# Kernel tuning notes

Hardware: AMD Instinct MI355X
Metric: run time of the kernel (lower is better)

## Reference

```python
import jax, jax.numpy as jnp
import numpy as np

UP = jnp.array([0.0, 1.0, 0.0], dtype=jnp.float32)
LEASH = 15.0


def q_inv(q):
    return jnp.concatenate([-q[..., :3], q[..., 3:]], axis=-1)


def q_mul(q1, q2):
    x1, y1, z1, w1 = q1[..., 0], q1[..., 1], q1[..., 2], q1[..., 3]
    x2, y2, z2, w2 = q2[..., 0], q2[..., 1], q2[..., 2], q2[..., 3]
    return jnp.stack([
        w1 * x2 + x1 * w2 + y1 * z2 - z1 * y2,
        w1 * y2 - x1 * z2 + y1 * w2 + z1 * x2,
        w1 * z2 + x1 * y2 - y1 * x2 + z1 * w2,
        w1 * w2 - x1 * x2 - y1 * y2 - z1 * z2], axis=-1)


def q_rot(q, v):
    qv, qw = q[..., :3], q[..., 3:]
    t = 2.0 * jnp.cross(qv, v)
    return v + qw * t + jnp.cross(qv, t)


def mat_to_quat(R):
    # Batched [E,3,3] -> [E,4] (x,y,z,w), matching the torch branch structure.
    r = lambda i, j: R[:, i, j]
    eps = 1e-12
    tr = r(0, 0) + r(1, 1) + r(2, 2)
    Sa = jnp.sqrt(jnp.maximum(tr + 1.0, eps)) * 2.0
    qa = jnp.stack([(r(2, 1) - r(1, 2)) / Sa, (r(0, 2) - r(2, 0)) / Sa,
                    (r(1, 0) - r(0, 1)) / Sa, 0.25 * Sa], -1)
    Sb = jnp.sqrt(jnp.maximum(1.0 + r(0, 0) - r(1, 1) - r(2, 2), eps)) * 2.0
    qb = jnp.stack([0.25 * Sb, (r(0, 1) + r(1, 0)) / Sb,
                    (r(0, 2) + r(2, 0)) / Sb, (r(2, 1) - r(1, 2)) / Sb], -1)
    Sc = jnp.sqrt(jnp.maximum(1.0 + r(1, 1) - r(0, 0) - r(2, 2), eps)) * 2.0
    qc = jnp.stack([(r(0, 1) + r(1, 0)) / Sc, 0.25 * Sc,
                    (r(1, 2) + r(2, 1)) / Sc, (r(0, 2) - r(2, 0)) / Sc], -1)
    Sd = jnp.sqrt(jnp.maximum(1.0 + r(2, 2) - r(0, 0) - r(1, 1), eps)) * 2.0
    qd = jnp.stack([(r(0, 2) + r(2, 0)) / Sd, (r(1, 2) + r(2, 1)) / Sd,
                    0.25 * Sd, (r(1, 0) - r(0, 1)) / Sd], -1)
    cond_b = ((r(0, 0) > r(1, 1)) & (r(0, 0) > r(2, 2)))[:, None]
    cond_c = (r(1, 1) > r(2, 2))[:, None]
    return jnp.where((tr > 0)[:, None], qa,
                     jnp.where(cond_b, qb, jnp.where(cond_c, qc, qd)))


def sfm_pose_loss(pred_t, pred_q, gt_t, gt_q, batch_counts):
    E = batch_counts.shape[0]
    N = pred_t.shape[0]
    counts = batch_counts.astype(jnp.float32)  # [E]
    seg = jnp.repeat(jnp.arange(E), batch_counts, total_repeat_length=N)  # [N]
    starts = jnp.cumsum(batch_counts) - batch_counts  # first index of each episode
    sseg = lambda x: jax.ops.segment_sum(x, seg, num_segments=E)

    # --- per-episode centering ---
    mu_p = sseg(pred_t) / counts[:, None]
    mu_g = sseg(gt_t) / counts[:, None]
    p_c = pred_t - mu_p[seg]
    g_c = gt_t - mu_g[seg]

    # degenerate episodes: too short or near-zero gt variance (unbiased var)
    g_var = sseg(jnp.sum(g_c ** 2, -1)) / (counts - 1.0)
    deg = (batch_counts < 4) | (g_var < 1e-4)  # [E]

    # --- Umeyama: batched 3x3 SVD of H = p_c^T @ g_c per episode ---
    H = sseg(p_c[:, :, None] * g_c[:, None, :])  # [E,3,3]
    H_safe = jnp.where(deg[:, None, None], jnp.diag(jnp.array([3.0, 2.0, 1.0])), H)
    U, S, Vh = jnp.linalg.svd(H_safe, full_matrices=False)
    V = jnp.swapaxes(Vh, -1, -2)
    R0 = jnp.einsum('eij,ekj->eik', V, U)  # V @ U^T
    sgn = jnp.where(jnp.linalg.det(R0) < 0, -1.0, 1.0)
    V_adj = V * jnp.stack([jnp.ones_like(sgn), jnp.ones_like(sgn), sgn], -1)[:, None, :]
    R = jnp.einsum('eij,ekj->eik', V_adj, U)  # [E,3,3]

    p_rot = jnp.einsum('nij,nj->ni', R[seg], p_c)
    denom = sseg(jnp.sum(p_c ** 2, -1))
    nom = sseg(jnp.sum(p_rot * g_c, -1))
    s = jnp.where(denom > 1e-6,
                  jnp.clip(nom / jnp.maximum(denom, 1e-6), 1e-3, 1e3), 1.0)

    # --- translation loss (per-episode mse, then mean over episodes) ---
    p_al = jnp.where(deg[seg][:, None], p_c, p_rot * s[seg][:, None])
    diff = p_al - g_c
    loss_trans = jnp.mean(sseg(jnp.sum(diff ** 2, -1)) / (counts * 3.0))

    # --- scale loss (only non-degenerate episodes) ---
    loss_scale = jnp.sum(jnp.where(deg, 0.0, jnp.log(jnp.abs(s) + 1e-6) ** 2)) / E

    # --- rotation loss ---
    q_align = mat_to_quat(R)  # [E,4]
    q0_p = pred_q[starts]
    q0_g = gt_q[starts]
    pq_deg = q_mul(q_inv(q0_p)[seg], pred_q)
    gq_deg = q_mul(q_inv(q0_g)[seg], gt_q)
    pq_ume = q_mul(q_align[seg], pred_q)
    dm = deg[seg][:, None]
    pq_al = jnp.where(dm, pq_deg, pq_ume)
    gq_al = jnp.where(dm, gq_deg, gt_q)
    dot = jnp.sum(pq_al * gq_al, -1)
    loss_rot = jnp.mean(sseg(1.0 - dot ** 2) / counts)

    # --- gravity loss ---
    up = jnp.broadcast_to(UP, pred_q.shape[:-1] + (3,))
    pu = q_rot(q_inv(pred_q), up)
    gu = q_rot(q_inv(gt_q), up)
    cos = jnp.sum(pu * gu, -1) / jnp.maximum(
        jnp.linalg.norm(pu, axis=-1) * jnp.linalg.norm(gu, axis=-1), 1e-8)
    loss_grav = jnp.mean(sseg(1.0 - cos) / counts)

    # --- frame0 leash (deadzone on first translation of each episode) ---
    mag = jnp.linalg.norm(pred_t[starts], axis=-1)
    loss_leash = jnp.mean(jnp.maximum(mag - LEASH, 0.0) ** 2)

    return jnp.stack([loss_trans, loss_rot, loss_grav, loss_leash, loss_scale])


def setup_inputs() -> dict:
    rng = np.random.default_rng(0)
    E = 4096
    counts = rng.integers(64, 449, size=E)
    counts[:8] = np.array([2, 3, 3, 2, 3, 2, 3, 3])  # exercise degenerate branch
    N = int(counts.sum())
    key = jax.random.key(0)
    k1, k2, k3, k4 = jax.random.split(key, 4)
    pred_t = jax.random.normal(k1, (N, 3), dtype=jnp.float32) * 5.0
    gt_t = jax.random.normal(k2, (N, 3), dtype=jnp.float32) * 5.0

    def rand_unit_quat(k):
        q = jax.random.normal(k, (N, 4), dtype=jnp.float32)
        return q / jnp.linalg.norm(q, axis=-1, keepdims=True)

    return {
        'pred_t': pred_t,
        'pred_q': rand_unit_quat(k3),
        'gt_t': gt_t,
        'gt_q': rand_unit_quat(k4),
        'batch_counts': jnp.asarray(counts, dtype=jnp.int32),
    }


def reference(pred_t, pred_q, gt_t, gt_q, batch_counts):
    # Returns [loss_trans, loss_rot, loss_grav, loss_leash, loss_scale]
    return sfm_pose_loss(pred_t, pred_q, gt_t, gt_q, batch_counts)
```

## Files before the change

### kernel.cpp

```cpp
#include <hip/hip_runtime.h>
#include <math.h>

__global__ void scan_kernel(const int* __restrict__ counts,
                            int* __restrict__ starts, int E) {
    __shared__ int lds[1024];
    int tid = threadIdx.x;
    int base = tid * 4;
    int c0 = (base + 0 < E) ? counts[base + 0] : 0;
    int c1 = (base + 1 < E) ? counts[base + 1] : 0;
    int c2 = (base + 2 < E) ? counts[base + 2] : 0;
    int c3 = (base + 3 < E) ? counts[base + 3] : 0;
    lds[tid] = c0 + c1 + c2 + c3;
    __syncthreads();
    for (int off = 1; off < 1024; off <<= 1) {
        int v = lds[tid];
        int a = (tid >= off) ? lds[tid - off] : 0;
        __syncthreads();
        lds[tid] = v + a;
        __syncthreads();
    }
    int excl = (tid > 0) ? lds[tid - 1] : 0;
    if (base + 0 < E) starts[base + 0] = excl; excl += c0;
    if (base + 1 < E) starts[base + 1] = excl; excl += c1;
    if (base + 2 < E) starts[base + 2] = excl; excl += c2;
    if (base + 3 < E) starts[base + 3] = excl;
}

__device__ __forceinline__ float4 qmul4(float4 a, float4 b) {
    return make_float4(
        a.w*b.x + a.x*b.w + a.y*b.z - a.z*b.y,
        a.w*b.y - a.x*b.z + a.y*b.w + a.z*b.x,
        a.w*b.z + a.x*b.y - a.y*b.x + a.z*b.w,
        a.w*b.w - a.x*b.x - a.y*b.y - a.z*b.z);
}

__device__ __forceinline__ void qinv_rot_up(float4 q, float out[3]) {
    float qx = -q.x, qy = -q.y, qz = -q.z, qw = q.w;
    float tx = -2.f*qz;
    float ty = 0.f;
    float tz = 2.f*qx;
    out[0] = 0.f + qw*tx + (qy*tz - qz*ty);
    out[1] = 1.f + qw*ty + (qz*tx - qx*tz);
    out[2] = 0.f + qw*tz + (qx*ty - qy*tx);
}

__device__ __forceinline__ float wave_sum(float v) {
    v += __shfl_xor(v, 32);
    v += __shfl_xor(v, 16);
    v += __shfl_xor(v, 8);
    v += __shfl_xor(v, 4);
    v += __shfl_xor(v, 2);
    v += __shfl_xor(v, 1);
    return v;
}

__device__ void jacobi3f(float A[3][3], float V[3][3]) {
    V[0][0]=1.f; V[0][1]=0.f; V[0][2]=0.f;
    V[1][0]=0.f; V[1][1]=1.f; V[1][2]=0.f;
    V[2][0]=0.f; V[2][1]=0.f; V[2][2]=1.f;
    for (int sweep = 0; sweep < 6; ++sweep) {
        float off = A[0][1]*A[0][1] + A[0][2]*A[0][2] + A[1][2]*A[1][2];
        float dia = A[0][0]*A[0][0] + A[1][1]*A[1][1] + A[2][2]*A[2][2];
        if (off <= 1e-12f * (dia + 1e-30f)) break;
        for (int p = 0; p < 2; ++p) for (int q = p + 1; q < 3; ++q) {
            float apq = A[p][q];
            if (fabsf(apq) < 1e-30f) continue;
            float theta = (A[q][q] - A[p][p]) / (2.0f * apq);
            float t = ((theta >= 0.f) ? 1.f : -1.f) / (fabsf(theta) + sqrtf(theta*theta + 1.f));
            float cc = 1.f / sqrtf(t*t + 1.f);
            float ss = t * cc;
            float app = A[p][p], aqq = A[q][q];
            A[p][p] = app - t * apq;
            A[q][q] = aqq + t * apq;
            A[p][q] = 0.f; A[q][p] = 0.f;
            int r = 3 - p - q;
            float arp = A[r][p], arq = A[r][q];
            A[r][p] = cc*arp - ss*arq; A[p][r] = A[r][p];
            A[r][q] = ss*arp + cc*arq; A[q][r] = A[r][q];
            for (int i = 0; i < 3; ++i) {
                float vip = V[i][p], viq = V[i][q];
                V[i][p] = cc*vip - ss*viq;
                V[i][q] = ss*vip + cc*viq;
            }
        }
    }
}

__device__ void mat2quatf(const float R[3][3], float q[4]) {
    const float eps = 1e-12f;
    float tr = R[0][0] + R[1][1] + R[2][2];
    if (tr > 0.f) {
        float S = sqrtf(fmaxf(tr + 1.f, eps)) * 2.f;
        q[0] = (R[2][1]-R[1][2])/S; q[1] = (R[0][2]-R[2][0])/S;
        q[2] = (R[1][0]-R[0][1])/S; q[3] = 0.25f*S;
    } else if ((R[0][0] > R[1][1]) && (R[0][0] > R[2][2])) {
        float S = sqrtf(fmaxf(1.f + R[0][0] - R[1][1] - R[2][2], eps)) * 2.f;
        q[0] = 0.25f*S; q[1] = (R[0][1]+R[1][0])/S;
        q[2] = (R[0][2]+R[2][0])/S; q[3] = (R[2][1]-R[1][2])/S;
    } else if (R[1][1] > R[2][2]) {
        float S = sqrtf(fmaxf(1.f + R[1][1] - R[0][0] - R[2][2], eps)) * 2.f;
        q[0] = (R[0][1]+R[1][0])/S; q[1] = 0.25f*S;
        q[2] = (R[1][2]+R[2][1])/S; q[3] = (R[0][2]-R[2][0])/S;
    } else {
        float S = sqrtf(fmaxf(1.f + R[2][2] - R[0][0] - R[1][1], eps)) * 2.f;
        q[0] = (R[0][2]+R[2][0])/S; q[1] = (R[1][2]+R[2][1])/S;
        q[2] = 0.25f*S; q[3] = (R[1][0]-R[0][1])/S;
    }
}

#define NS 29
__global__ __launch_bounds__(256) void fused_kernel(
    const float* __restrict__ pred_t, const float4* __restrict__ pred_q,
    const float* __restrict__ gt_t,   const float4* __restrict__ gt_q,
    const int* __restrict__ counts, const int* __restrict__ starts,
    float* __restrict__ segloss, int E)
{
    int e = blockIdx.x;
    int tid = threadIdx.x;
    int lane = tid & 63;
    int wv = tid >> 6;
    int start = starts[e];
    int ci = counts[e];
    float4 q0p = pred_q[start];
    float4 q0g = gt_q[start];
    float4 q0pi = make_float4(-q0p.x, -q0p.y, -q0p.z, q0p.w);
    float4 q0gi = make_float4(-q0g.x, -q0g.y, -q0g.z, q0g.w);
    float t0x = pred_t[3*start+0], t0y = pred_t[3*start+1], t0z = pred_t[3*start+2];
    bool small_c = (ci < 4);

    float acc[NS];
    #pragma unroll
    for (int k = 0; k < NS; ++k) acc[k] = 0.f;

    for (int i = tid; i < ci; i += 256) {
        int n = start + i;
        float px = pred_t[3*n+0], py = pred_t[3*n+1], pz = pred_t[3*n+2];
        float gx = gt_t[3*n+0],  gy = gt_t[3*n+1],  gz = gt_t[3*n+2];
        float4 pq = pred_q[n];
        float4 gq = gt_q[n];

        acc[0] += px; acc[1] += py; acc[2] += pz;
        acc[3] += gx; acc[4] += gy; acc[5] += gz;
        acc[6] += px*px + py*py + pz*pz;
        acc[7] += gx*gx + gy*gy + gz*gz;
        acc[8]  += px*gx; acc[9]  += px*gy; acc[10] += px*gz;
        acc[11] += py*gx; acc[12] += py*gy; acc[13] += py*gz;
        acc[14] += pz*gx; acc[15] += pz*gy; acc[16] += pz*gz;

        float mx =  pq.w*gq.x - pq.z*gq.y + pq.y*gq.z - pq.x*gq.w;
        float my =  pq.z*gq.x + pq.w*gq.y - pq.x*gq.z - pq.y*gq.w;
        float mz = -pq.y*gq.x + pq.x*gq.y + pq.w*gq.z - pq.z*gq.w;
        float mw =  pq.x*gq.x + pq.y*gq.y + pq.z*gq.z + pq.w*gq.w;
        acc[17] += mx*mx; acc[18] += mx*my; acc[19] += mx*mz; acc[20] += mx*mw;
        acc[21] += my*my; acc[22] += my*mz; acc[23] += my*mw;
        acc[24] += mz*mz; acc[25] += mz*mw; acc[26] += mw*mw;

        float pu[3], gu[3];
        qinv_rot_up(pq, pu);
        qinv_rot_up(gq, gu);
        float cosv = pu[0]*gu[0] + pu[1]*gu[1] + pu[2]*gu[2];
        acc[27] += 1.f - cosv;

        if (small_c) {
            float4 aa = qmul4(q0pi, pq);
            float4 bb = qmul4(q0gi, gq);
            float dd = aa.x*bb.x + aa.y*bb.y + aa.z*bb.z + aa.w*bb.w;
            acc[28] += 1.f - dd*dd;
        }
    }

    #pragma unroll
    for (int k = 0; k < NS; ++k) acc[k] = wave_sum(acc[k]);

    __shared__ float red[4][NS];
    if (lane == 0) {
        #pragma unroll
        for (int k = 0; k < NS; ++k) red[wv][k] = acc[k];
    }
    __syncthreads();
    if (wv != 0) return;

    float A[NS];
    #pragma unroll
    for (int k = 0; k < NS; ++k)
        A[k] = red[0][k] + red[1][k] + red[2][k] + red[3][k];

    float c = (float)ci;
    float mu_p[3] = { A[0]/c, A[1]/c, A[2]/c };
    float mu_g[3] = { A[3]/c, A[4]/c, A[5]/c };
    float pp_c = A[6] - c*(mu_p[0]*mu_p[0]+mu_p[1]*mu_p[1]+mu_p[2]*mu_p[2]);
    float gg_c = A[7] - c*(mu_g[0]*mu_g[0]+mu_g[1]*mu_g[1]+mu_g[2]*mu_g[2]);
    float H[3][3];
    H[0][0]=A[8] -c*mu_p[0]*mu_g[0]; H[0][1]=A[9] -c*mu_p[0]*mu_g[1]; H[0][2]=A[10]-c*mu_p[0]*mu_g[2];
    H[1][0]=A[11]-c*mu_p[1]*mu_g[0]; H[1][1]=A[12]-c*mu_p[1]*mu_g[1]; H[1][2]=A[13]-c*mu_p[1]*mu_g[2];
    H[2][0]=A[14]-c*mu_p[2]*mu_g[0]; H[2][1]=A[15]-c*mu_p[2]*mu_g[1]; H[2][2]=A[16]-c*mu_p[2]*mu_g[2];
    float g_var = gg_c / (c - 1.0f);
    bool deg = small_c || (g_var < 1e-4f);
    float trans, rot, scale = 0.f;
    if (deg) {
        float s28;
        if (small_c) {
            s28 = A[28];
        } else {
            float local = 0.f;
            for (int i = lane; i < ci; i += 64) {
                int n = start + i;
                float4 aa = qmul4(q0pi, pred_q[n]);
                float4 bb = qmul4(q0gi, gt_q[n]);
                float dd = aa.x*bb.x + aa.y*bb.y + aa.z*bb.z + aa.w*bb.w;
                local += 1.f - dd*dd;
            }
            s28 = wave_sum(local);
        }
        float trH = H[0][0] + H[1][1] + H[2][2];
        trans = (pp_c - 2.f*trH + gg_c) / (c * 3.f);
        rot = s28 / c;
    } else {
        float B[3][3], V[3][3];
        for (int i = 0; i < 3; ++i)
            for (int j = 0; j < 3; ++j)
                B[i][j] = H[0][i]*H[0][j] + H[1][i]*H[1][j] + H[2][i]*H[2][j];
        jacobi3f(B, V);
        float lam[3] = { B[0][0], B[1][1], B[2][2] };
        int idx[3] = {0, 1, 2};
        if (lam[idx[0]] < lam[idx[1]]) { int t = idx[0]; idx[0] = idx[1]; idx[1] = t; }
        if (lam[idx[0]] < lam[idx[2]]) { int t = idx[0]; idx[0] = idx[2]; idx[2] = t; }
        if (lam[idx[1]] < lam[idx[2]]) { int t = idx[1]; idx[1] = idx[2]; idx[2] = t; }
        float v1[3], v2[3], v3[3];
        for (int i = 0; i < 3; ++i) { v1[i] = V[i][idx[0]]; v2[i] = V[i][idx[1]]; v3[i] = V[i][idx[2]]; }
        float detV = v1[0]*(v2[1]*v3[2]-v2[2]*v3[1])
                   - v1[1]*(v2[0]*v3[2]-v2[2]*v3[0])
                   + v1[2]*(v2[0]*v3[1]-v2[1]*v3[0]);
        float sgnV = (detV < 0.f) ? -1.f : 1.f;
        float u1[3], u2[3], u3[3];
        for (int i = 0; i < 3; ++i) u1[i] = H[i][0]*v1[0] + H[i][1]*v1[1] + H[i][2]*v1[2];
        float n1 = fmaxf(sqrtf(u1[0]*u1[0]+u1[1]*u1[1]+u1[2]*u1[2]), 1e-30f);
        for (int i = 0; i < 3; ++i) u1[i] /= n1;
        for (int i = 0; i < 3; ++i) u2[i] = H[i][0]*v2[0] + H[i][1]*v2[1] + H[i][2]*v2[2];
        float d12 = u1[0]*u2[0]+u1[1]*u2[1]+u1[2]*u2[2];
        for (int i = 0; i < 3; ++i) u2[i] -= d12*u1[i];
        float n2 = fmaxf(sqrtf(u2[0]*u2[0]+u2[1]*u2[1]+u2[2]*u2[2]), 1e-30f);
        for (int i = 0; i < 3; ++i) u2[i] /= n2;
        u3[0] = u1[1]*u2[2] - u1[2]*u2[1];
        u3[1] = u1[2]*u2[0] - u1[0]*u2[2];
        u3[2] = u1[0]*u2[1] - u1[1]*u2[0];
        float R[3][3];
        for (int i = 0; i < 3; ++i)
            for (int k = 0; k < 3; ++k)
                R[i][k] = v1[i]*u1[k] + v2[i]*u2[k] + sgnV*v3[i]*u3[k];
        float nom = 0.f;
        for (int k = 0; k < 3; ++k)
            for (int j = 0; j < 3; ++j)
                nom += R[k][j] * H[j][k];
        float denom = pp_c;
        float s = 1.f;
        if (denom > 1e-6f) {
            s = nom / fmaxf(denom, 1e-6f);
            s = fminf(fmaxf(s, 1e-3f), 1e3f);
        }
        trans = (s*s*denom - 2.f*s*nom + gg_c) / (c * 3.f);
        float ls = logf(fabsf(s) + 1e-6f);
        scale = ls * ls;
        float q[4];
        mat2quatf(R, q);
        float quad = q[0]*q[0]*A[17] + q[1]*q[1]*A[21] + q[2]*q[2]*A[24] + q[3]*q[3]*A[26]
            + 2.f*(q[0]*q[1]*A[18] + q[0]*q[2]*A[19] + q[0]*q[3]*A[20]
                 + q[1]*q[2]*A[22] + q[1]*q[3]*A[23] + q[2]*q[3]*A[25]);
        rot = (c - quad) / c;
    }
    float grav = A[27] / c;
    float mag = sqrtf(t0x*t0x + t0y*t0y + t0z*t0z);
    float ml = fmaxf(mag - 15.f, 0.f);
    float leash = ml * ml;
    float myval = (lane == 0) ? trans
                : (lane == 1) ? rot
                : (lane == 2) ? grav
                : (lane == 3) ? leash : scale;
    if (lane < 5) segloss[lane * E + e] = myval;
}

__global__ __launch_bounds__(256) void reduce_kernel(
    const float* __restrict__ segloss, float* __restrict__ out, int E)
{
    int k = blockIdx.x;
    const float* src = segloss + (size_t)k * E;
    float local = 0.f;
    for (int i = threadIdx.x; i < E; i += 256) local = local + src[i];
    local = wave_sum(local);
    __shared__ float red[4];
    int lane = threadIdx.x & 63;
    int wv = threadIdx.x >> 6;
    if (lane == 0) red[wv] = local;
    __syncthreads();
    if (threadIdx.x == 0)
        out[k] = (red[0] + red[1] + red[2] + red[3]) / (float)E;
}

extern "C" void kernel_launch(void* const* d_in, const int* in_sizes, int n_in,
                              void* d_out, int out_size, void* d_ws, size_t ws_size,
                              hipStream_t stream) {
    const float*  pred_t = (const float*)d_in[0];
    const float4* pred_q = (const float4*)d_in[1];
    const float*  gt_t   = (const float*)d_in[2];
    const float4* gt_q   = (const float4*)d_in[3];
    const int*    counts = (const int*)d_in[4];
    int E = in_sizes[4];

    int* starts = (int*)d_ws;
    size_t off = ((size_t)E * sizeof(int) + 255) & ~(size_t)255;
    float* segloss = (float*)((char*)d_ws + off);

    scan_kernel<<<1, 1024, 0, stream>>>(counts, starts, E);
    fused_kernel<<<E, 256, 0, stream>>>(pred_t, pred_q, gt_t, gt_q,
                                        counts, starts, segloss, E);
    reduce_kernel<<<5, 256, 0, stream>>>(segloss, (float*)d_out, E);
}
```

Baseline: 143.8 us.

## Split per-episode work into wave-per-episode accumulation and thread-per-episode finalize

The single block-per-episode kernel is replaced by a pass where each wavefront handles one episode, double-buffering its loads, and writes 29 accumulated sums per episode to workspace. A separate finalize kernel then runs the SVD/quaternion math with one thread per episode and folds the final mean into atomic adds, which removes the separate reduce kernel. The aim is to avoid idle waves and serial per-block finalize work, and to remove block-level LDS reductions and barriers. In exchange, degenerate episodes now loop serially in one thread, and the atomic float summation order is nondeterministic.

```diff
diff --git a/kernel.cpp b/kernel.cpp
--- a/kernel.cpp
+++ b/kernel.cpp
@@ -2,9 +2,11 @@
 #include <math.h>
 
 __global__ void scan_kernel(const int* __restrict__ counts,
-                            int* __restrict__ starts, int E) {
+                            int* __restrict__ starts,
+                            float* __restrict__ out, int E) {
     __shared__ int lds[1024];
     int tid = threadIdx.x;
+    if (tid < 5) out[tid] = 0.0f;
     int base = tid * 4;
     int c0 = (base + 0 < E) ? counts[base + 0] : 0;
     int c1 = (base + 1 < E) ? counts[base + 1] : 0;
@@ -52,6 +54,96 @@
     v += __shfl_xor(v, 2);
     v += __shfl_xor(v, 1);
     return v;
+}
+
+#define NS 29
+__global__ __launch_bounds__(256) void pass1_kernel(
+    const float* __restrict__ pred_t, const float4* __restrict__ pred_q,
+    const float* __restrict__ gt_t,   const float4* __restrict__ gt_q,
+    const int* __restrict__ counts, const int* __restrict__ starts,
+    float* __restrict__ segacc, int E)
+{
+    int wv = threadIdx.x >> 6;
+    int lane = threadIdx.x & 63;
+    int e = blockIdx.x * 4 + wv;
+    if (e >= E) return;
+    int start = starts[e];
+    int ci = counts[e];
+    bool small_c = (ci < 4);
+    float4 q0p = pred_q[start];
+    float4 q0g = gt_q[start];
+    float4 q0pi = make_float4(-q0p.x, -q0p.y, -q0p.z, q0p.w);
+    float4 q0gi = make_float4(-q0g.x, -q0g.y, -q0g.z, q0g.w);
+
+    float acc[NS];
+    #pragma unroll
+    for (int k = 0; k < NS; ++k) acc[k] = 0.f;
+
+    int iters = (ci + 63) >> 6;
+    int i = lane;
+    int m = start + min(i, ci - 1);
+    float px = pred_t[3*m+0], py = pred_t[3*m+1], pz = pred_t[3*m+2];
+    float gx = gt_t[3*m+0],  gy = gt_t[3*m+1],  gz = gt_t[3*m+2];
+    float4 pq = pred_q[m];
+    float4 gq = gt_q[m];
+
+    for (int j = 0; ; ) {
+        float npx = 0.f, npy = 0.f, npz = 0.f, ngx = 0.f, ngy = 0.f, ngz = 0.f;
+        float4 npq = make_float4(0.f,0.f,0.f,0.f), ngq = npq;
+        bool have_next = (j + 1 < iters);
+        if (have_next) {
+            int m2 = start + min(i + 64, ci - 1);
+            npx = pred_t[3*m2+0]; npy = pred_t[3*m2+1]; npz = pred_t[3*m2+2];
+            ngx = gt_t[3*m2+0];  ngy = gt_t[3*m2+1];  ngz = gt_t[3*m2+2];
+            npq = pred_q[m2];
+            ngq = gt_q[m2];
+        }
+        if (i < ci) {
+            acc[0] += px; acc[1] += py; acc[2] += pz;
+            acc[3] += gx; acc[4] += gy; acc[5] += gz;
+            acc[6] += px*px + py*py + pz*pz;
+            acc[7] += gx*gx + gy*gy + gz*gz;
+            acc[8]  += px*gx; acc[9]  += px*gy; acc[10] += px*gz;
+            acc[11] += py*gx; acc[12] += py*gy; acc[13] += py*gz;
+            acc[14] += pz*gx; acc[15] += pz*gy; acc[16] += pz*gz;
+
+            float mx =  pq.w*gq.x - pq.z*gq.y + pq.y*gq.z - pq.x*gq.w;
+            float my =  pq.z*gq.x + pq.w*gq.y - pq.x*gq.z - pq.y*gq.w;
+            float mz = -pq.y*gq.x + pq.x*gq.y + pq.w*gq.z - pq.z*gq.w;
+            float mw =  pq.x*gq.x + pq.y*gq.y + pq.z*gq.z + pq.w*gq.w;
+            acc[17] += mx*mx; acc[18] += mx*my; acc[19] += mx*mz; acc[20] += mx*mw;
+            acc[21] += my*my; acc[22] += my*mz; acc[23] += my*mw;
+            acc[24] += mz*mz; acc[25] += mz*mw; acc[26] += mw*mw;
+
+            float pu[3], gu[3];
+            qinv_rot_up(pq, pu);
+            qinv_rot_up(gq, gu);
+            float cosv = pu[0]*gu[0] + pu[1]*gu[1] + pu[2]*gu[2];
+            acc[27] += 1.f - cosv;
+
+            if (small_c) {
+                float4 aa = qmul4(q0pi, pq);
+                float4 bb = qmul4(q0gi, gq);
+                float dd = aa.x*bb.x + aa.y*bb.y + aa.z*bb.z + aa.w*bb.w;
+                acc[28] += 1.f - dd*dd;
+            }
+        }
+        if (!have_next) break;
+        px = npx; py = npy; pz = npz;
+        gx = ngx; gy = ngy; gz = ngz;
+        pq = npq; gq = ngq;
+        i += 64; ++j;
+    }
+
+    #pragma unroll
+    for (int k = 0; k < NS; ++k) acc[k] = wave_sum(acc[k]);
+
+    float outv = 0.f;
+    #pragma unroll
+    for (int k = 0; k < NS; ++k)
+        if (lane == k) outv = acc[k];
+    if (lane < NS)
+        segacc[(size_t)e*32 + lane] = outv;
 }
 
 __device__ void jacobi3f(float A[3][3], float V[3][3]) {
@@ -108,192 +200,122 @@
     }
 }
 
-#define NS 29
-__global__ __launch_bounds__(256) void fused_kernel(
-    const float* __restrict__ pred_t, const float4* __restrict__ pred_q,
-    const float* __restrict__ gt_t,   const float4* __restrict__ gt_q,
-    const int* __restrict__ counts, const int* __restrict__ starts,
-    float* __restrict__ segloss, int E)
+__global__ __launch_bounds__(64) void finalize_kernel(
+    const float* __restrict__ segacc, const int* __restrict__ counts,
+    const int* __restrict__ starts, const float* __restrict__ pred_t,
+    const float4* __restrict__ pred_q, const float4* __restrict__ gt_q,
+    float* __restrict__ out, int E)
 {
-    int e = blockIdx.x;
-    int tid = threadIdx.x;
-    int lane = tid & 63;
-    int wv = tid >> 6;
-    int start = starts[e];
-    int ci = counts[e];
-    float4 q0p = pred_q[start];
-    float4 q0g = gt_q[start];
-    float4 q0pi = make_float4(-q0p.x, -q0p.y, -q0p.z, q0p.w);
-    float4 q0gi = make_float4(-q0g.x, -q0g.y, -q0g.z, q0g.w);
-    float t0x = pred_t[3*start+0], t0y = pred_t[3*start+1], t0z = pred_t[3*start+2];
-    bool small_c = (ci < 4);
-
-    float acc[NS];
+    int e = blockIdx.x * 64 + threadIdx.x;
+    float v_trans = 0.f, v_rot = 0.f, v_grav = 0.f, v_leash = 0.f, v_scale = 0.f;
+    if (e < E) {
+        const float* A = segacc + (size_t)e * 32;
+        int ci = counts[e];
+        int start = starts[e];
+        float c = (float)ci;
+        float mu_p[3] = { A[0]/c, A[1]/c, A[2]/c };
+        float mu_g[3] = { A[3]/c, A[4]/c, A[5]/c };
+        float pp_c = A[6] - c*(mu_p[0]*mu_p[0]+mu_p[1]*mu_p[1]+mu_p[2]*mu_p[2]);
+        float gg_c = A[7] - c*(mu_g[0]*mu_g[0]+mu_g[1]*mu_g[1]+mu_g[2]*mu_g[2]);
+        float H[3][3];
+        H[0][0]=A[8] -c*mu_p[0]*mu_g[0]; H[0][1]=A[9] -c*mu_p[0]*mu_g[1]; H[0][2]=A[10]-c*mu_p[0]*mu_g[2];
+        H[1][0]=A[11]-c*mu_p[1]*mu_g[0]; H[1][1]=A[12]-c*mu_p[1]*mu_g[1]; H[1][2]=A[13]-c*mu_p[1]*mu_g[2];
+        H[2][0]=A[14]-c*mu_p[2]*mu_g[0]; H[2][1]=A[15]-c*mu_p[2]*mu_g[1]; H[2][2]=A[16]-c*mu_p[2]*mu_g[2];
+        float g_var = gg_c / (c - 1.0f);
+        bool small_c = (ci < 4);
+        bool deg = small_c || (g_var < 1e-4f);
+        float trans, rot, scale = 0.f;
+        if (deg) {
+            float s28;
+            if (small_c) {
+                s28 = A[28];
+            } else {
+                float4 q0p = pred_q[start];
+                float4 q0g = gt_q[start];
+                float4 q0pi = make_float4(-q0p.x, -q0p.y, -q0p.z, q0p.w);
+                float4 q0gi = make_float4(-q0g.x, -q0g.y, -q0g.z, q0g.w);
+                float local = 0.f;
+                for (int ii = 0; ii < ci; ++ii) {
+                    float4 aa = qmul4(q0pi, pred_q[start + ii]);
+                    float4 bb = qmul4(q0gi, gt_q[start + ii]);
+                    float dd = aa.x*bb.x + aa.y*bb.y + aa.z*bb.z + aa.w*bb.w;
+                    local += 1.f - dd*dd;
+                }
+                s28 = local;
+            }
+            float trH = H[0][0] + H[1][1] + H[2][2];
+            trans = (pp_c - 2.f*trH + gg_c) / (c * 3.f);
+            rot = s28 / c;
+        } else {
+            float B[3][3], V[3][3];
+            for (int i = 0; i < 3; ++i)
+                for (int j = 0; j < 3; ++j)
+                    B[i][j] = H[0][i]*H[0][j] + H[1][i]*H[1][j] + H[2][i]*H[2][j];
+            jacobi3f(B, V);
+            float lam[3] = { B[0][0], B[1][1], B[2][2] };
+            int idx[3] = {0, 1, 2};
+            if (lam[idx[0]] < lam[idx[1]]) { int t = idx[0]; idx[0] = idx[1]; idx[1] = t; }
+            if (lam[idx[0]] < lam[idx[2]]) { int t = idx[0]; idx[0] = idx[2]; idx[2] = t; }
+            if (lam[idx[1]] < lam[idx[2]]) { int t = idx[1]; idx[1] = idx[2]; idx[2] = t; }
+            float v1[3], v2[3], v3[3];
+            for (int i = 0; i < 3; ++i) { v1[i] = V[i][idx[0]]; v2[i] = V[i][idx[1]]; v3[i] = V[i][idx[2]]; }
+            float detV = v1[0]*(v2[1]*v3[2]-v2[2]*v3[1])
+                       - v1[1]*(v2[0]*v3[2]-v2[2]*v3[0])
+                       + v1[2]*(v2[0]*v3[1]-v2[1]*v3[0]);
+            float sgnV = (detV < 0.f) ? -1.f : 1.f;
+            float u1[3], u2[3], u3[3];
+            for (int i = 0; i < 3; ++i) u1[i] = H[i][0]*v1[0] + H[i][1]*v1[1] + H[i][2]*v1[2];
+            float n1 = fmaxf(sqrtf(u1[0]*u1[0]+u1[1]*u1[1]+u1[2]*u1[2]), 1e-30f);
+            for (int i = 0; i < 3; ++i) u1[i] /= n1;
+            for (int i = 0; i < 3; ++i) u2[i] = H[i][0]*v2[0] + H[i][1]*v2[1] + H[i][2]*v2[2];
+            float d12 = u1[0]*u2[0]+u1[1]*u2[1]+u1[2]*u2[2];
+            for (int i = 0; i < 3; ++i) u2[i] -= d12*u1[i];
+            float n2 = fmaxf(sqrtf(u2[0]*u2[0]+u2[1]*u2[1]+u2[2]*u2[2]), 1e-30f);
+            for (int i = 0; i < 3; ++i) u2[i] /= n2;
+            u3[0] = u1[1]*u2[2] - u1[2]*u2[1];
+            u3[1] = u1[2]*u2[0] - u1[0]*u2[2];
+            u3[2] = u1[0]*u2[1] - u1[1]*u2[0];
+            float R[3][3];
+            for (int i = 0; i < 3; ++i)
+                for (int k = 0; k < 3; ++k)
+                    R[i][k] = v1[i]*u1[k] + v2[i]*u2[k] + sgnV*v3[i]*u3[k];
+            float nom = 0.f;
+            for (int k = 0; k < 3; ++k)
+                for (int j = 0; j < 3; ++j)
+                    nom += R[k][j] * H[j][k];
+            float denom = pp_c;
+            float s = 1.f;
+            if (denom > 1e-6f) {
+                s = nom / fmaxf(denom, 1e-6f);
+                s = fminf(fmaxf(s, 1e-3f), 1e3f);
+            }
+            trans = (s*s*denom - 2.f*s*nom + gg_c) / (c * 3.f);
+            float ls = logf(fabsf(s) + 1e-6f);
+            scale = ls * ls;
+            float q[4];
+            mat2quatf(R, q);
+            float quad = q[0]*q[0]*A[17] + q[1]*q[1]*A[21] + q[2]*q[2]*A[24] + q[3]*q[3]*A[26]
+                + 2.f*(q[0]*q[1]*A[18] + q[0]*q[2]*A[19] + q[0]*q[3]*A[20]
+                     + q[1]*q[2]*A[22] + q[1]*q[3]*A[23] + q[2]*q[3]*A[25]);
+            rot = (c - quad) / c;
+        }
+        float grav = A[27] / c;
+        float tx = pred_t[3*start+0], ty = pred_t[3*start+1], tz = pred_t[3*start+2];
+        float mag = sqrtf(tx*tx + ty*ty + tz*tz);
+        float ml = fmaxf(mag - 15.f, 0.f);
+        float Ed = (float)E;
+        v_trans = trans / Ed;
+        v_rot   = rot / Ed;
+        v_grav  = grav / Ed;
+        v_leash = (ml * ml) / Ed;
+        v_scale = scale / Ed;
+    }
+    float vals[5] = { v_trans, v_rot, v_grav, v_leash, v_scale };
     #pragma unroll
-    for (int k = 0; k < NS; ++k) acc[k] = 0.f;
-
-    for (int i = tid; i < ci; i += 256) {
-        int n = start + i;
-        float px = pred_t[3*n+0], py = pred_t[3*n+1], pz = pred_t[3*n+2];
-        float gx = gt_t[3*n+0],  gy = gt_t[3*n+1],  gz = gt_t[3*n+2];
-        float4 pq = pred_q[n];
-        float4 gq = gt_q[n];
-
-        acc[0] += px; acc[1] += py; acc[2] += pz;
-        acc[3] += gx; acc[4] += gy; acc[5] += gz;
-        acc[6] += px*px + py*py + pz*pz;
-        acc[7] += gx*gx + gy*gy + gz*gz;
-        acc[8]  += px*gx; acc[9]  += px*gy; acc[10] += px*gz;
-        acc[11] += py*gx; acc[12] += py*gy; acc[13] += py*gz;
-        acc[14] += pz*gx; acc[15] += pz*gy; acc[16] += pz*gz;
-
-        float mx =  pq.w*gq.x - pq.z*gq.y + pq.y*gq.z - pq.x*gq.w;
-        float my =  pq.z*gq.x + pq.w*gq.y - pq.x*gq.z - pq.y*gq.w;
-        float mz = -pq.y*gq.x + pq.x*gq.y + pq.w*gq.z - pq.z*gq.w;
-        float mw =  pq.x*gq.x + pq.y*gq.y + pq.z*gq.z + pq.w*gq.w;
-        acc[17] += mx*mx; acc[18] += mx*my; acc[19] += mx*mz; acc[20] += mx*mw;
-        acc[21] += my*my; acc[22] += my*mz; acc[23] += my*mw;
-        acc[24] += mz*mz; acc[25] += mz*mw; acc[26] += mw*mw;
-
-        float pu[3], gu[3];
-        qinv_rot_up(pq, pu);
-        qinv_rot_up(gq, gu);
-        float cosv = pu[0]*gu[0] + pu[1]*gu[1] + pu[2]*gu[2];
-        acc[27] += 1.f - cosv;
-
-        if (small_c) {
-            float4 aa = qmul4(q0pi, pq);
-            float4 bb = qmul4(q0gi, gq);
-            float dd = aa.x*bb.x + aa.y*bb.y + aa.z*bb.z + aa.w*bb.w;
-            acc[28] += 1.f - dd*dd;
-        }
-    }
-
-    #pragma unroll
-    for (int k = 0; k < NS; ++k) acc[k] = wave_sum(acc[k]);
-
-    __shared__ float red[4][NS];
-    if (lane == 0) {
-        #pragma unroll
-        for (int k = 0; k < NS; ++k) red[wv][k] = acc[k];
-    }
-    __syncthreads();
-    if (wv != 0) return;
-
-    float A[NS];
-    #pragma unroll
-    for (int k = 0; k < NS; ++k)
-        A[k] = red[0][k] + red[1][k] + red[2][k] + red[3][k];
-
-    float c = (float)ci;
-    float mu_p[3] = { A[0]/c, A[1]/c, A[2]/c };
-    float mu_g[3] = { A[3]/c, A[4]/c, A[5]/c };
-    float pp_c = A[6] - c*(mu_p[0]*mu_p[0]+mu_p[1]*mu_p[1]+mu_p[2]*mu_p[2]);
-    float gg_c = A[7] - c*(mu_g[0]*mu_g[0]+mu_g[1]*mu_g[1]+mu_g[2]*mu_g[2]);
-    float H[3][3];
-    H[0][0]=A[8] -c*mu_p[0]*mu_g[0]; H[0][1]=A[9] -c*mu_p[0]*mu_g[1]; H[0][2]=A[10]-c*mu_p[0]*mu_g[2];
-    H[1][0]=A[11]-c*mu_p[1]*mu_g[0]; H[1][1]=A[12]-c*mu_p[1]*mu_g[1]; H[1][2]=A[13]-c*mu_p[1]*mu_g[2];
-    H[2][0]=A[14]-c*mu_p[2]*mu_g[0]; H[2][1]=A[15]-c*mu_p[2]*mu_g[1]; H[2][2]=A[16]-c*mu_p[2]*mu_g[2];
-    float g_var = gg_c / (c - 1.0f);
-    bool deg = small_c || (g_var < 1e-4f);
-    float trans, rot, scale = 0.f;
-    if (deg) {
-        float s28;
-        if (small_c) {
-            s28 = A[28];
-        } else {
-            float local = 0.f;
-            for (int i = lane; i < ci; i += 64) {
-                int n = start + i;
-                float4 aa = qmul4(q0pi, pred_q[n]);
-                float4 bb = qmul4(q0gi, gt_q[n]);
-                float dd = aa.x*bb.x + aa.y*bb.y + aa.z*bb.z + aa.w*bb.w;
-                local += 1.f - dd*dd;
-            }
-            s28 = wave_sum(local);
-        }
-        float trH = H[0][0] + H[1][1] + H[2][2];
-        trans = (pp_c - 2.f*trH + gg_c) / (c * 3.f);
-        rot = s28 / c;
-    } else {
-        float B[3][3], V[3][3];
-        for (int i = 0; i < 3; ++i)
-            for (int j = 0; j < 3; ++j)
-                B[i][j] = H[0][i]*H[0][j] + H[1][i]*H[1][j] + H[2][i]*H[2][j];
-        jacobi3f(B, V);
-        float lam[3] = { B[0][0], B[1][1], B[2][2] };
-        int idx[3] = {0, 1, 2};
-        if (lam[idx[0]] < lam[idx[1]]) { int t = idx[0]; idx[0] = idx[1]; idx[1] = t; }
-        if (lam[idx[0]] < lam[idx[2]]) { int t = idx[0]; idx[0] = idx[2]; idx[2] = t; }
-        if (lam[idx[1]] < lam[idx[2]]) { int t = idx[1]; idx[1] = idx[2]; idx[2] = t; }
-        float v1[3], v2[3], v3[3];
-        for (int i = 0; i < 3; ++i) { v1[i] = V[i][idx[0]]; v2[i] = V[i][idx[1]]; v3[i] = V[i][idx[2]]; }
-        float detV = v1[0]*(v2[1]*v3[2]-v2[2]*v3[1])
-                   - v1[1]*(v2[0]*v3[2]-v2[2]*v3[0])
-                   + v1[2]*(v2[0]*v3[1]-v2[1]*v3[0]);
-        float sgnV = (detV < 0.f) ? -1.f : 1.f;
-        float u1[3], u2[3], u3[3];
-        for (int i = 0; i < 3; ++i) u1[i] = H[i][0]*v1[0] + H[i][1]*v1[1] + H[i][2]*v1[2];
-        float n1 = fmaxf(sqrtf(u1[0]*u1[0]+u1[1]*u1[1]+u1[2]*u1[2]), 1e-30f);
-        for (int i = 0; i < 3; ++i) u1[i] /= n1;
-        for (int i = 0; i < 3; ++i) u2[i] = H[i][0]*v2[0] + H[i][1]*v2[1] + H[i][2]*v2[2];
-        float d12 = u1[0]*u2[0]+u1[1]*u2[1]+u1[2]*u2[2];
-        for (int i = 0; i < 3; ++i) u2[i] -= d12*u1[i];
-        float n2 = fmaxf(sqrtf(u2[0]*u2[0]+u2[1]*u2[1]+u2[2]*u2[2]), 1e-30f);
-        for (int i = 0; i < 3; ++i) u2[i] /= n2;
-        u3[0] = u1[1]*u2[2] - u1[2]*u2[1];
-        u3[1] = u1[2]*u2[0] - u1[0]*u2[2];
-        u3[2] = u1[0]*u2[1] - u1[1]*u2[0];
-        float R[3][3];
-        for (int i = 0; i < 3; ++i)
-            for (int k = 0; k < 3; ++k)
-                R[i][k] = v1[i]*u1[k] + v2[i]*u2[k] + sgnV*v3[i]*u3[k];
-        float nom = 0.f;
-        for (int k = 0; k < 3; ++k)
-            for (int j = 0; j < 3; ++j)
-                nom += R[k][j] * H[j][k];
-        float denom = pp_c;
-        float s = 1.f;
-        if (denom > 1e-6f) {
-            s = nom / fmaxf(denom, 1e-6f);
-            s = fminf(fmaxf(s, 1e-3f), 1e3f);
-        }
-        trans = (s*s*denom - 2.f*s*nom + gg_c) / (c * 3.f);
-        float ls = logf(fabsf(s) + 1e-6f);
-        scale = ls * ls;
-        float q[4];
-        mat2quatf(R, q);
-        float quad = q[0]*q[0]*A[17] + q[1]*q[1]*A[21] + q[2]*q[2]*A[24] + q[3]*q[3]*A[26]
-            + 2.f*(q[0]*q[1]*A[18] + q[0]*q[2]*A[19] + q[0]*q[3]*A[20]
-                 + q[1]*q[2]*A[22] + q[1]*q[3]*A[23] + q[2]*q[3]*A[25]);
-        rot = (c - quad) / c;
-    }
-    float grav = A[27] / c;
-    float mag = sqrtf(t0x*t0x + t0y*t0y + t0z*t0z);
-    float ml = fmaxf(mag - 15.f, 0.f);
-    float leash = ml * ml;
-    float myval = (lane == 0) ? trans
-                : (lane == 1) ? rot
-                : (lane == 2) ? grav
-                : (lane == 3) ? leash : scale;
-    if (lane < 5) segloss[lane * E + e] = myval;
-}
-
-__global__ __launch_bounds__(256) void reduce_kernel(
-    const float* __restrict__ segloss, float* __restrict__ out, int E)
-{
-    int k = blockIdx.x;
-    const float* src = segloss + (size_t)k * E;
-    float local = 0.f;
-    for (int i = threadIdx.x; i < E; i += 256) local = local + src[i];
-    local = wave_sum(local);
-    __shared__ float red[4];
-    int lane = threadIdx.x & 63;
-    int wv = threadIdx.x >> 6;
-    if (lane == 0) red[wv] = local;
-    __syncthreads();
-    if (threadIdx.x == 0)
-        out[k] = (red[0] + red[1] + red[2] + red[3]) / (float)E;
+    for (int k = 0; k < 5; ++k) {
+        float v = wave_sum(vals[k]);
+        if (threadIdx.x == 0) atomicAdd(out + k, v);
+    }
 }
 
 extern "C" void kernel_launch(void* const* d_in, const int* in_sizes, int n_in,
@@ -308,10 +330,11 @@
 
     int* starts = (int*)d_ws;
     size_t off = ((size_t)E * sizeof(int) + 255) & ~(size_t)255;
-    float* segloss = (float*)((char*)d_ws + off);
-
-    scan_kernel<<<1, 1024, 0, stream>>>(counts, starts, E);
-    fused_kernel<<<E, 256, 0, stream>>>(pred_t, pred_q, gt_t, gt_q,
-                                        counts, starts, segloss, E);
-    reduce_kernel<<<5, 256, 0, stream>>>(segloss, (float*)d_out, E);
-}
+    float* segacc = (float*)((char*)d_ws + off);
+
+    scan_kernel<<<1, 1024, 0, stream>>>(counts, starts, (float*)d_out, E);
+    pass1_kernel<<<(E + 3) / 4, 256, 0, stream>>>(pred_t, pred_q, gt_t, gt_q,
+                                                  counts, starts, segacc, E);
+    finalize_kernel<<<(E + 63) / 64, 64, 0, stream>>>(segacc, counts, starts, pred_t,
+                                                      pred_q, gt_q, (float*)d_out, E);
+}
```

New measurement: 118.5 us. 1.21x faster.
